# Optimization experiments

Hardware: AMD Instinct MI355X
Metric: run time of the kernel (lower is better)

The kernel has to match this reference:

```python
import jax, jax.numpy as jnp
import numpy as np

N, M, D, DV = 8192, 8192, 512, 512

def setup_inputs() -> dict:
    key = jax.random.key(0)
    kq, kk, kv = jax.random.split(key, 3)
    return {
        "query": jax.random.normal(kq, (N, D), dtype=jnp.float32),
        "key": jax.random.normal(kk, (M, D), dtype=jnp.float32),
        "value": jax.random.normal(kv, (M, DV), dtype=jnp.float32),
    }

def reference(query, key, value):
    # scores: [N, M] = Q @ K^T (no scale, no mask, matching the torch module)
    scores = query @ key.T
    attn = jax.nn.softmax(scores, axis=-1)
    return attn @ value
```

## Files before the change

kernel.cpp:

```cpp
#include <hip/hip_runtime.h>
#include <hip/hip_fp16.h>
#include <stdint.h>

typedef _Float16 f16;
typedef _Float16 f16x8 __attribute__((ext_vector_type(8)));
typedef float    f32x4 __attribute__((ext_vector_type(4)));
typedef int      i32x4 __attribute__((ext_vector_type(4)));

#define NQ 8192
#define NK 8192
#define DD 512
#define DVV 512

__device__ __forceinline__ void stage16(const void* g, void* ldsbase, int lane) {
#if __has_builtin(__builtin_amdgcn_global_load_lds)
  __builtin_amdgcn_global_load_lds((const __attribute__((address_space(1))) void*)g,
                                   (__attribute__((address_space(3))) void*)ldsbase, 16, 0, 0);
#else
  ((i32x4*)ldsbase)[lane] = *(const i32x4*)g;
#endif
}

__global__ void conv_hilo(const float* __restrict__ src, f16* __restrict__ hi,
                          f16* __restrict__ lo, int n8) {
  int i = blockIdx.x * 256 + threadIdx.x;
  if (i >= n8) return;
  const float4* s4 = (const float4*)src;
  float4 a = s4[2 * i], b = s4[2 * i + 1];
  float vv[8] = {a.x, a.y, a.z, a.w, b.x, b.y, b.z, b.w};
  f16 h8[8], l8[8];
#pragma unroll
  for (int j = 0; j < 8; ++j) {
    f16 h = (f16)vv[j];
    h8[j] = h;
    l8[j] = (f16)(vv[j] - (float)h);
  }
  *(f16x8*)(hi + (size_t)i * 8) = *(f16x8*)h8;
  *(f16x8*)(lo + (size_t)i * 8) = *(f16x8*)l8;
}

__global__ void conv_f16k(const float* __restrict__ src, f16* __restrict__ dst, int n8) {
  int i = blockIdx.x * 256 + threadIdx.x;
  if (i >= n8) return;
  const float4* s4 = (const float4*)src;
  float4 a = s4[2 * i], b = s4[2 * i + 1];
  float vv[8] = {a.x, a.y, a.z, a.w, b.x, b.y, b.z, b.w};
  f16 h8[8];
#pragma unroll
  for (int j = 0; j < 8; ++j) h8[j] = (f16)vv[j];
  *(f16x8*)(dst + (size_t)i * 8) = *(f16x8*)h8;
}

__global__ void conv_vT(const float* __restrict__ v, f16* __restrict__ vT) {
  __shared__ float t[64][65];
  int k0 = blockIdx.x * 64, d0 = blockIdx.y * 64;
#pragma unroll
  for (int e = 0; e < 16; ++e) {
    int idx = threadIdx.x + e * 256;
    int kr = idx >> 6, dc = idx & 63;
    t[kr][dc] = v[(size_t)(k0 + kr) * DVV + d0 + dc];
  }
  __syncthreads();
  int dl = threadIdx.x >> 2, seg = (threadIdx.x & 3) * 16;
  f16 tmp[16];
#pragma unroll
  for (int c = 0; c < 16; ++c) tmp[c] = (f16)t[seg + c][dl];
  f16* dst = vT + (size_t)(d0 + dl) * NK + k0 + seg;
  *(f16x8*)dst = *(f16x8*)tmp;
  *(f16x8*)(dst + 8) = *(f16x8*)(tmp + 8);
}

__global__ __launch_bounds__(512, 2) void qk_kernel(
    const f16* __restrict__ qhi, const f16* __restrict__ qlo,
    const f16* __restrict__ khi,
    f16* __restrict__ s16, float* __restrict__ pm, float* __restrict__ ps) {
  __shared__ f16 LS[3 * 3 * 8192];
  __shared__ float red[2][4][128];
  const int tid = threadIdx.x;
  const int lane = tid & 63, wid = tid >> 6;
  const int wr = wid >> 2, wc = wid & 3;
  const int bx = blockIdx.x, by = blockIdx.y;
  const int lo16 = lane & 15, hi4 = lane >> 4;
  const int swz = (lo16 & 3) ^ ((lo16 >> 2) & 3);
  const int u_s = hi4 ^ swz;

  f32x4 acc[8][4] = {};

  const f16* tp[3] = {qhi + (size_t)(by * 256) * DD, qlo + (size_t)(by * 256) * DD,
                      khi + (size_t)(bx * 256) * DD};
  const int srow4 = lane >> 2, usl = lane & 3;
  const f16* sptr[6];
  int dbase[6];
#pragma unroll
  for (int s2 = 0; s2 < 6; ++s2) {
    int u = wid + s2 * 8;
    int tt = u >> 4, rb = u & 15;
    int r = rb * 16 + srow4;
    int ug = usl ^ (r & 3) ^ ((r >> 2) & 3);
    sptr[s2] = tp[tt] + (size_t)r * DD + ug * 8;
    dbase[s2] = tt * 3 * 8192 + rb * 512;
  }
  f16* lsf = (f16*)LS;

#define STG(s2, t2, buf) stage16(sptr[s2] + (t2) * 32, lsf + dbase[s2] + (buf) * 8192, lane)

#pragma unroll
  for (int s2 = 0; s2 < 6; ++s2) STG(s2, 0, 0);
#pragma unroll
  for (int s2 = 0; s2 < 6; ++s2) STG(s2, 1, 1);
  asm volatile("s_waitcnt vmcnt(6)" ::: "memory");
  __builtin_amdgcn_s_barrier();
  asm volatile("" ::: "memory");

  const int abase = (wr * 128 + lo16) * 32 + u_s * 8;
  const int bbase = (wc * 64 + lo16) * 32 + u_s * 8;

  int cur = 0, pre = 2;
  for (int t = 0; t < 16; ++t) {
    const f16* Qh = lsf + cur * 8192;
    const f16* Ql = lsf + (3 + cur) * 8192;
    const f16* Kh = lsf + (6 + cur) * 8192;
    const bool st = (t <= 13);
    f16x8 bfr[4], ah[4], al[4];
#pragma unroll
    for (int j = 0; j < 4; ++j) bfr[j] = *(const f16x8*)&Kh[bbase + j * 512];
#pragma unroll
    for (int i = 0; i < 4; ++i) {
      ah[i] = *(const f16x8*)&Qh[abase + i * 512];
      al[i] = *(const f16x8*)&Ql[abase + i * 512];
    }
    if (st) { STG(0, t + 2, pre); STG(1, t + 2, pre); STG(2, t + 2, pre); }
    __builtin_amdgcn_s_barrier();
    asm volatile("" ::: "memory");
    __builtin_amdgcn_s_setprio(1);
#pragma unroll
    for (int i = 0; i < 4; ++i)
#pragma unroll
      for (int j = 0; j < 4; ++j) {
        acc[i][j] = __builtin_amdgcn_mfma_f32_16x16x32_f16(ah[i], bfr[j], acc[i][j], 0, 0, 0);
        acc[i][j] = __builtin_amdgcn_mfma_f32_16x16x32_f16(al[i], bfr[j], acc[i][j], 0, 0, 0);
      }
    __builtin_amdgcn_s_setprio(0);
    __builtin_amdgcn_s_barrier();
    asm volatile("" ::: "memory");
#pragma unroll
    for (int i = 0; i < 4; ++i) {
      ah[i] = *(const f16x8*)&Qh[abase + (4 + i) * 512];
      al[i] = *(const f16x8*)&Ql[abase + (4 + i) * 512];
    }
    if (st) { STG(3, t + 2, pre); STG(4, t + 2, pre); STG(5, t + 2, pre); }
    __builtin_amdgcn_s_barrier();
    asm volatile("" ::: "memory");
    __builtin_amdgcn_s_setprio(1);
#pragma unroll
    for (int i = 0; i < 4; ++i)
#pragma unroll
      for (int j = 0; j < 4; ++j) {
        acc[4 + i][j] = __builtin_amdgcn_mfma_f32_16x16x32_f16(ah[i], bfr[j], acc[4 + i][j], 0, 0, 0);
        acc[4 + i][j] = __builtin_amdgcn_mfma_f32_16x16x32_f16(al[i], bfr[j], acc[4 + i][j], 0, 0, 0);
      }
    __builtin_amdgcn_s_setprio(0);
    if (st) asm volatile("s_waitcnt vmcnt(6)" ::: "memory");
    else    asm volatile("s_waitcnt vmcnt(0)" ::: "memory");
    __builtin_amdgcn_s_barrier();
    asm volatile("" ::: "memory");
    cur = (cur == 2) ? 0 : cur + 1;
    pre = (pre == 2) ? 0 : pre + 1;
  }
#undef STG

  __syncthreads();
  float rmax[8][4];
#pragma unroll
  for (int i = 0; i < 8; ++i)
#pragma unroll
    for (int r = 0; r < 4; ++r) {
      float m = fmaxf(fmaxf(acc[i][0][r], acc[i][1][r]), fmaxf(acc[i][2][r], acc[i][3][r]));
#pragma unroll
      for (int d = 1; d < 16; d <<= 1) m = fmaxf(m, __shfl_xor(m, d, 64));
      rmax[i][r] = m;
    }
  if (lo16 == 0) {
#pragma unroll
    for (int i = 0; i < 8; ++i)
#pragma unroll
      for (int r = 0; r < 4; ++r) red[wr][wc][i * 16 + hi4 * 4 + r] = rmax[i][r];
  }
  __syncthreads();
  float pmv[8][4];
#pragma unroll
  for (int i = 0; i < 8; ++i)
#pragma unroll
    for (int r = 0; r < 4; ++r) {
      int rl = i * 16 + hi4 * 4 + r;
      pmv[i][r] = fmaxf(fmaxf(red[wr][0][rl], red[wr][1][rl]),
                        fmaxf(red[wr][2][rl], red[wr][3][rl]));
    }
  __syncthreads();
  float rsum[8][4];
#pragma unroll
  for (int i = 0; i < 8; ++i)
#pragma unroll
    for (int r = 0; r < 4; ++r) {
      float s = 0.f;
#pragma unroll
      for (int j = 0; j < 4; ++j) {
        float p = __expf(acc[i][j][r] - pmv[i][r]);
        acc[i][j][r] = p;
        s += p;
      }
#pragma unroll
      for (int d = 1; d < 16; d <<= 1) s += __shfl_xor(s, d, 64);
      rsum[i][r] = s;
    }
#pragma unroll
  for (int i = 0; i < 8; ++i)
#pragma unroll
    for (int r = 0; r < 4; ++r) {
      size_t grow = (size_t)(by * 256 + wr * 128 + i * 16 + hi4 * 4 + r);
#pragma unroll
      for (int j = 0; j < 4; ++j)
        s16[grow * NK + bx * 256 + wc * 64 + j * 16 + lo16] = (f16)acc[i][j][r];
    }
  if (lo16 == 0) {
#pragma unroll
    for (int i = 0; i < 8; ++i)
#pragma unroll
      for (int r = 0; r < 4; ++r) red[wr][wc][i * 16 + hi4 * 4 + r] = rsum[i][r];
  }
  __syncthreads();
  if (wc == 0 && lo16 == 0) {
#pragma unroll
    for (int i = 0; i < 8; ++i)
#pragma unroll
      for (int r = 0; r < 4; ++r) {
        int rl = i * 16 + hi4 * 4 + r;
        size_t grow = (size_t)(by * 256 + wr * 128 + rl);
        pm[grow * 32 + bx] = pmv[i][r];
        ps[grow * 32 + bx] = red[wr][0][rl] + red[wr][1][rl] + red[wr][2][rl] + red[wr][3][rl];
      }
  }
}

__global__ void red_kernel(const float* __restrict__ pm, const float* __restrict__ ps,
                           float* __restrict__ coef) {
  int row = blockIdx.x * 8 + (threadIdx.x >> 5);
  int t = threadIdx.x & 31;
  float pmt = pm[(size_t)row * 32 + t];
  float m = pmt;
#pragma unroll
  for (int d = 1; d < 32; d <<= 1) m = fmaxf(m, __shfl_xor(m, d, 32));
  float e = __expf(pmt - m);
  float l = ps[(size_t)row * 32 + t] * e;
#pragma unroll
  for (int d = 1; d < 32; d <<= 1) l += __shfl_xor(l, d, 32);
  coef[(size_t)row * 32 + t] = e / l;
}

__global__ __launch_bounds__(256, 2) void pv_kernel(
    const f16* __restrict__ p16, const float* __restrict__ coef,
    const f16* __restrict__ vT, float* __restrict__ dst,
    int steps, size_t zstride) {
  __shared__ f16 lsA[2][128 * 64];
  __shared__ f16 lsB[2][128 * 64];
  const int tid = threadIdx.x, lane = tid & 63, wid = tid >> 6;
  const int lo16 = lane & 15, hi4 = lane >> 4;
  const int wr = wid >> 1, wc = wid & 1;
  const int bx = blockIdx.x, by = blockIdx.y, bz = blockIdx.z;
  const int g0 = bz * steps;
  f32x4 acc[4][4] = {};

  const int arow0 = tid >> 3, acol = tid & 7;
  const int srw = lane >> 3;
  const int sc = (lane & 7) ^ srw;

  f16x8 va[4];
  float scv[4];

#pragma unroll
  for (int u = 0; u < 4; ++u)
    va[u] = *(const f16x8*)(p16 + (size_t)(by * 128 + u * 32 + arow0) * NK + (size_t)g0 * 64 + acol * 8);
#pragma unroll
  for (int i = 0; i < 4; ++i) {
    int unit = wid * 4 + i;
    int row = unit * 8 + srw;
    stage16(vT + (size_t)(bx * 128 + row) * NK + (size_t)g0 * 64 + sc * 8,
            &lsB[0][unit * 512], lane);
  }
#pragma unroll
  for (int u = 0; u < 4; ++u)
    scv[u] = coef[(size_t)(by * 128 + u * 32 + arow0) * 32 + (g0 >> 2)];
#pragma unroll
  for (int u = 0; u < 4; ++u) {
    int row = u * 32 + arow0;
    f16x8 vv = va[u] * (f16)scv[u];
    *(f16x8*)&lsA[0][row * 64 + ((acol ^ (row & 7)) << 3)] = vv;
  }
  __syncthreads();

  for (int s = 0; s < steps; ++s) {
    const int cur = s & 1, nxt = cur ^ 1;
    const int g = g0 + s;
    if (s + 1 < steps) {
#pragma unroll
      for (int u = 0; u < 4; ++u)
        va[u] = *(const f16x8*)(p16 + (size_t)(by * 128 + u * 32 + arow0) * NK +
                                (size_t)(g + 1) * 64 + acol * 8);
#pragma unroll
      for (int i = 0; i < 4; ++i) {
        int unit = wid * 4 + i;
        int row = unit * 8 + srw;
        stage16(vT + (size_t)(bx * 128 + row) * NK + (size_t)(g + 1) * 64 + sc * 8,
                &lsB[nxt][unit * 512], lane);
      }
#pragma unroll
      for (int u = 0; u < 4; ++u)
        scv[u] = coef[(size_t)(by * 128 + u * 32 + arow0) * 32 + ((g + 1) >> 2)];
    }
#pragma unroll
    for (int ks = 0; ks < 2; ++ks) {
      f16x8 af[4], bf[4];
#pragma unroll
      for (int i = 0; i < 4; ++i) {
        int row = wr * 64 + i * 16 + lo16;
        af[i] = *(const f16x8*)&lsA[cur][row * 64 + (((ks * 4 + hi4) ^ (row & 7)) << 3)];
      }
#pragma unroll
      for (int j = 0; j < 4; ++j) {
        int dv = wc * 64 + j * 16 + lo16;
        bf[j] = *(const f16x8*)&lsB[cur][dv * 64 + (((ks * 4 + hi4) ^ (dv & 7)) << 3)];
      }
#pragma unroll
      for (int i = 0; i < 4; ++i)
#pragma unroll
        for (int j = 0; j < 4; ++j)
          acc[i][j] = __builtin_amdgcn_mfma_f32_16x16x32_f16(af[i], bf[j], acc[i][j], 0, 0, 0);
    }
    if (s + 1 < steps) {
#pragma unroll
      for (int u = 0; u < 4; ++u) {
        int row = u * 32 + arow0;
        f16x8 vv = va[u] * (f16)scv[u];
        *(f16x8*)&lsA[nxt][row * 64 + ((acol ^ (row & 7)) << 3)] = vv;
      }
    }
    __syncthreads();
  }

  float* o = dst + (size_t)bz * zstride;
#pragma unroll
  for (int i = 0; i < 4; ++i)
#pragma unroll
    for (int j = 0; j < 4; ++j)
#pragma unroll
      for (int r = 0; r < 4; ++r)
        o[(size_t)(by * 128 + wr * 64 + i * 16 + hi4 * 4 + r) * DVV +
          bx * 128 + wc * 64 + j * 16 + lo16] = acc[i][j][r];
}

__global__ void reduce_out(const float* __restrict__ part, float* __restrict__ out,
                           int ks, size_t n4) {
  size_t i = (size_t)blockIdx.x * 256 + threadIdx.x;
  if (i >= n4) return;
  float4 a = ((const float4*)part)[i];
  for (int z = 1; z < ks; ++z) {
    float4 b = ((const float4*)(part + z * n4 * 4))[i];
    a.x += b.x; a.y += b.y; a.z += b.z; a.w += b.w;
  }
  ((float4*)out)[i] = a;
}

__global__ void zero_out(float* o, int n) {
  int i = blockIdx.x * 256 + threadIdx.x;
  if (i < n) o[i] = 0.f;
}

extern "C" void kernel_launch(void* const* d_in, const int* in_sizes, int n_in,
                              void* d_out, int out_size, void* d_ws, size_t ws_size,
                              hipStream_t stream) {
  (void)in_sizes; (void)n_in; (void)out_size;
  const float* Q = (const float*)d_in[0];
  const float* K = (const float*)d_in[1];
  const float* V = (const float*)d_in[2];
  float* out = (float*)d_out;

  const size_t sz16 = (size_t)NK * DD * 2;
  const size_t fixedB = 2 * sz16;
  const size_t perRow = 1024 * 2 + 128 * 3 + (size_t)NK * 2;
  const size_t partB = (size_t)16384 * DVV * 4;
  int nc = 0;
  for (int cand = 8192; cand >= 1024; cand >>= 1)
    if (fixedB + (size_t)cand * perRow + partB <= ws_size) { nc = cand; break; }
  if (nc == 0) {
    zero_out<<<(NQ * DVV + 255) / 256, 256, 0, stream>>>(out, NQ * DVV);
    return;
  }
  const int ks = 16384 / nc;
  const int steps = 128 / ks;

  char* w = (char*)d_ws;
  f16* khi = (f16*)w;
  f16* vT = (f16*)(w + sz16);
  char* p = w + fixedB;
  f16* qhi = (f16*)p;      p += (size_t)nc * 1024;
  f16* qlo = (f16*)p;      p += (size_t)nc * 1024;
  float* pm = (float*)p;   p += (size_t)nc * 128;
  float* ps = (float*)p;   p += (size_t)nc * 128;
  float* coef = (float*)p; p += (size_t)nc * 128;
  f16* s16 = (f16*)p;      p += (size_t)nc * NK * 2;
  float* part = (float*)p;

  conv_f16k<<<NK * DD / 8 / 256, 256, 0, stream>>>(K, khi, NK * DD / 8);
  conv_vT<<<dim3(NK / 64, DVV / 64), 256, 0, stream>>>(V, vT);

  for (int c = 0; c < NQ / nc; ++c) {
    conv_hilo<<<nc * DD / 8 / 256, 256, 0, stream>>>(Q + (size_t)c * nc * DD, qhi, qlo, nc * DD / 8);
    qk_kernel<<<dim3(NK / 256, nc / 256), 512, 0, stream>>>(qhi, qlo, khi, s16, pm, ps);
    red_kernel<<<nc / 8, 256, 0, stream>>>(pm, ps, coef);
    pv_kernel<<<dim3(DVV / 128, nc / 128, ks), 256, 0, stream>>>(
        s16, coef, vT, part, steps, (size_t)nc * DVV);
    reduce_out<<<(int)(((size_t)nc * DVV / 4 + 255) / 256), 256, 0, stream>>>(
        part, out + (size_t)c * nc * DVV, ks, (size_t)nc * DVV / 4);
  }
}
```

Before: 303.5 us.

## Drop Q hi/lo split, use plain fp16 Q and restructure QK staging

Removes the hi/lo fp16 split of Q, so QK^T uses a single fp16 product instead of two MFMAs per tile pair. The QK main loop moves from a 3-buffer, 32-wide K-step pipeline to a 2-buffer, 64-wide K-step pipeline with an XOR-swizzled LDS layout. This halves the QK MFMA work and the Q conversion traffic. It gives up the extra precision in the scores, which get exponentiated without scaling, so accuracy near tolerance is at risk.

```diff
diff --git a/kernel.cpp b/kernel.cpp
--- a/kernel.cpp
+++ b/kernel.cpp
@@ -21,24 +21,6 @@
 #endif
 }
 
-__global__ void conv_hilo(const float* __restrict__ src, f16* __restrict__ hi,
-                          f16* __restrict__ lo, int n8) {
-  int i = blockIdx.x * 256 + threadIdx.x;
-  if (i >= n8) return;
-  const float4* s4 = (const float4*)src;
-  float4 a = s4[2 * i], b = s4[2 * i + 1];
-  float vv[8] = {a.x, a.y, a.z, a.w, b.x, b.y, b.z, b.w};
-  f16 h8[8], l8[8];
-#pragma unroll
-  for (int j = 0; j < 8; ++j) {
-    f16 h = (f16)vv[j];
-    h8[j] = h;
-    l8[j] = (f16)(vv[j] - (float)h);
-  }
-  *(f16x8*)(hi + (size_t)i * 8) = *(f16x8*)h8;
-  *(f16x8*)(lo + (size_t)i * 8) = *(f16x8*)l8;
-}
-
 __global__ void conv_f16k(const float* __restrict__ src, f16* __restrict__ dst, int n8) {
   int i = blockIdx.x * 256 + threadIdx.x;
   if (i >= n8) return;
@@ -71,105 +53,90 @@
 }
 
 __global__ __launch_bounds__(512, 2) void qk_kernel(
-    const f16* __restrict__ qhi, const f16* __restrict__ qlo,
-    const f16* __restrict__ khi,
+    const f16* __restrict__ q16, const f16* __restrict__ k16,
     f16* __restrict__ s16, float* __restrict__ pm, float* __restrict__ ps) {
-  __shared__ f16 LS[3 * 3 * 8192];
+  __shared__ f16 LS[2 * 2 * 16384];
   __shared__ float red[2][4][128];
-  const int tid = threadIdx.x;
-  const int lane = tid & 63, wid = tid >> 6;
+  const int tid = threadIdx.x, lane = tid & 63, wid = tid >> 6;
   const int wr = wid >> 2, wc = wid & 3;
   const int bx = blockIdx.x, by = blockIdx.y;
   const int lo16 = lane & 15, hi4 = lane >> 4;
-  const int swz = (lo16 & 3) ^ ((lo16 >> 2) & 3);
-  const int u_s = hi4 ^ swz;
 
   f32x4 acc[8][4] = {};
 
-  const f16* tp[3] = {qhi + (size_t)(by * 256) * DD, qlo + (size_t)(by * 256) * DD,
-                      khi + (size_t)(bx * 256) * DD};
-  const int srow4 = lane >> 2, usl = lane & 3;
-  const f16* sptr[6];
-  int dbase[6];
-#pragma unroll
-  for (int s2 = 0; s2 < 6; ++s2) {
-    int u = wid + s2 * 8;
-    int tt = u >> 4, rb = u & 15;
-    int r = rb * 16 + srow4;
-    int ug = usl ^ (r & 3) ^ ((r >> 2) & 3);
-    sptr[s2] = tp[tt] + (size_t)r * DD + ug * 8;
-    dbase[s2] = tt * 3 * 8192 + rb * 512;
-  }
-  f16* lsf = (f16*)LS;
-
-#define STG(s2, t2, buf) stage16(sptr[s2] + (t2) * 32, lsf + dbase[s2] + (buf) * 8192, lane)
-
-#pragma unroll
-  for (int s2 = 0; s2 < 6; ++s2) STG(s2, 0, 0);
-#pragma unroll
-  for (int s2 = 0; s2 < 6; ++s2) STG(s2, 1, 1);
-  asm volatile("s_waitcnt vmcnt(6)" ::: "memory");
+  const int srw = lane >> 3, sc8 = (lane & 7) ^ srw;
+  const f16* aptr[4]; const f16* bptr[4]; int adst[4], bdst[4];
+#pragma unroll
+  for (int u = 0; u < 4; ++u) {
+    int r = wid * 32 + u * 8 + srw;
+    aptr[u] = q16 + (size_t)(by * 256 + r) * DD + sc8 * 8;
+    bptr[u] = k16 + (size_t)(bx * 256 + r) * DD + sc8 * 8;
+    adst[u] = (wid * 32 + u * 8) * 64;
+    bdst[u] = adst[u] + 16384;
+  }
+  int aoff[8][2], boff[4][2];
+#pragma unroll
+  for (int m = 0; m < 8; ++m)
+#pragma unroll
+    for (int kk = 0; kk < 2; ++kk) {
+      int row = wr * 128 + m * 16 + lo16;
+      aoff[m][kk] = row * 64 + (((kk * 4 + hi4) ^ (row & 7)) << 3);
+    }
+#pragma unroll
+  for (int n = 0; n < 4; ++n)
+#pragma unroll
+    for (int kk = 0; kk < 2; ++kk) {
+      int row = wc * 64 + n * 16 + lo16;
+      boff[n][kk] = 16384 + row * 64 + (((kk * 4 + hi4) ^ (row & 7)) << 3);
+    }
+
+#define STG(t2, buf)                                                        \
+  do {                                                                      \
+    _Pragma("unroll") for (int u = 0; u < 4; ++u) {                         \
+      stage16(aptr[u] + (t2) * 64, LS + (buf) * 32768 + adst[u], lane);     \
+      stage16(bptr[u] + (t2) * 64, LS + (buf) * 32768 + bdst[u], lane);     \
+    }                                                                       \
+  } while (0)
+
+  STG(0, 0);
+  asm volatile("s_waitcnt vmcnt(0)" ::: "memory");
   __builtin_amdgcn_s_barrier();
   asm volatile("" ::: "memory");
 
-  const int abase = (wr * 128 + lo16) * 32 + u_s * 8;
-  const int bbase = (wc * 64 + lo16) * 32 + u_s * 8;
-
-  int cur = 0, pre = 2;
-  for (int t = 0; t < 16; ++t) {
-    const f16* Qh = lsf + cur * 8192;
-    const f16* Ql = lsf + (3 + cur) * 8192;
-    const f16* Kh = lsf + (6 + cur) * 8192;
-    const bool st = (t <= 13);
-    f16x8 bfr[4], ah[4], al[4];
-#pragma unroll
-    for (int j = 0; j < 4; ++j) bfr[j] = *(const f16x8*)&Kh[bbase + j * 512];
-#pragma unroll
-    for (int i = 0; i < 4; ++i) {
-      ah[i] = *(const f16x8*)&Qh[abase + i * 512];
-      al[i] = *(const f16x8*)&Ql[abase + i * 512];
-    }
-    if (st) { STG(0, t + 2, pre); STG(1, t + 2, pre); STG(2, t + 2, pre); }
+  for (int t = 0; t < 8; ++t) {
+    const int cur = t & 1;
+    if (t < 7) STG(t + 1, cur ^ 1);
+    const f16* Bb = LS + cur * 32768;
+    f16x8 bf[2][4];
+#pragma unroll
+    for (int n = 0; n < 4; ++n)
+#pragma unroll
+      for (int kk = 0; kk < 2; ++kk) bf[kk][n] = *(const f16x8*)&Bb[boff[n][kk]];
+#pragma unroll
+    for (int h = 0; h < 2; ++h) {
+      f16x8 af[4][2];
+#pragma unroll
+      for (int mi = 0; mi < 4; ++mi)
+#pragma unroll
+        for (int kk = 0; kk < 2; ++kk) af[mi][kk] = *(const f16x8*)&Bb[aoff[h * 4 + mi][kk]];
+      __builtin_amdgcn_s_setprio(1);
+#pragma unroll
+      for (int mi = 0; mi < 4; ++mi)
+#pragma unroll
+        for (int n = 0; n < 4; ++n) {
+          acc[h * 4 + mi][n] =
+              __builtin_amdgcn_mfma_f32_16x16x32_f16(af[mi][0], bf[0][n], acc[h * 4 + mi][n], 0, 0, 0);
+          acc[h * 4 + mi][n] =
+              __builtin_amdgcn_mfma_f32_16x16x32_f16(af[mi][1], bf[1][n], acc[h * 4 + mi][n], 0, 0, 0);
+        }
+      __builtin_amdgcn_s_setprio(0);
+    }
+    asm volatile("s_waitcnt vmcnt(0)" ::: "memory");
     __builtin_amdgcn_s_barrier();
     asm volatile("" ::: "memory");
-    __builtin_amdgcn_s_setprio(1);
-#pragma unroll
-    for (int i = 0; i < 4; ++i)
-#pragma unroll
-      for (int j = 0; j < 4; ++j) {
-        acc[i][j] = __builtin_amdgcn_mfma_f32_16x16x32_f16(ah[i], bfr[j], acc[i][j], 0, 0, 0);
-        acc[i][j] = __builtin_amdgcn_mfma_f32_16x16x32_f16(al[i], bfr[j], acc[i][j], 0, 0, 0);
-      }
-    __builtin_amdgcn_s_setprio(0);
-    __builtin_amdgcn_s_barrier();
-    asm volatile("" ::: "memory");
-#pragma unroll
-    for (int i = 0; i < 4; ++i) {
-      ah[i] = *(const f16x8*)&Qh[abase + (4 + i) * 512];
-      al[i] = *(const f16x8*)&Ql[abase + (4 + i) * 512];
-    }
-    if (st) { STG(3, t + 2, pre); STG(4, t + 2, pre); STG(5, t + 2, pre); }
-    __builtin_amdgcn_s_barrier();
-    asm volatile("" ::: "memory");
-    __builtin_amdgcn_s_setprio(1);
-#pragma unroll
-    for (int i = 0; i < 4; ++i)
-#pragma unroll
-      for (int j = 0; j < 4; ++j) {
-        acc[4 + i][j] = __builtin_amdgcn_mfma_f32_16x16x32_f16(ah[i], bfr[j], acc[4 + i][j], 0, 0, 0);
-        acc[4 + i][j] = __builtin_amdgcn_mfma_f32_16x16x32_f16(al[i], bfr[j], acc[4 + i][j], 0, 0, 0);
-      }
-    __builtin_amdgcn_s_setprio(0);
-    if (st) asm volatile("s_waitcnt vmcnt(6)" ::: "memory");
-    else    asm volatile("s_waitcnt vmcnt(0)" ::: "memory");
-    __builtin_amdgcn_s_barrier();
-    asm volatile("" ::: "memory");
-    cur = (cur == 2) ? 0 : cur + 1;
-    pre = (pre == 2) ? 0 : pre + 1;
   }
 #undef STG
 
-  __syncthreads();
   float rmax[8][4];
 #pragma unroll
   for (int i = 0; i < 8; ++i)
@@ -386,7 +353,7 @@
 
   const size_t sz16 = (size_t)NK * DD * 2;
   const size_t fixedB = 2 * sz16;
-  const size_t perRow = 1024 * 2 + 128 * 3 + (size_t)NK * 2;
+  const size_t perRow = 1024 + 128 * 3 + (size_t)NK * 2;
   const size_t partB = (size_t)16384 * DVV * 4;
   int nc = 0;
   for (int cand = 8192; cand >= 1024; cand >>= 1)
@@ -399,23 +366,22 @@
   const int steps = 128 / ks;
 
   char* w = (char*)d_ws;
-  f16* khi = (f16*)w;
+  f16* k16 = (f16*)w;
   f16* vT = (f16*)(w + sz16);
   char* p = w + fixedB;
-  f16* qhi = (f16*)p;      p += (size_t)nc * 1024;
-  f16* qlo = (f16*)p;      p += (size_t)nc * 1024;
+  f16* q16 = (f16*)p;      p += (size_t)nc * 1024;
   float* pm = (float*)p;   p += (size_t)nc * 128;
   float* ps = (float*)p;   p += (size_t)nc * 128;
   float* coef = (float*)p; p += (size_t)nc * 128;
   f16* s16 = (f16*)p;      p += (size_t)nc * NK * 2;
   float* part = (float*)p;
 
-  conv_f16k<<<NK * DD / 8 / 256, 256, 0, stream>>>(K, khi, NK * DD / 8);
+  conv_f16k<<<NK * DD / 8 / 256, 256, 0, stream>>>(K, k16, NK * DD / 8);
   conv_vT<<<dim3(NK / 64, DVV / 64), 256, 0, stream>>>(V, vT);
 
   for (int c = 0; c < NQ / nc; ++c) {
-    conv_hilo<<<nc * DD / 8 / 256, 256, 0, stream>>>(Q + (size_t)c * nc * DD, qhi, qlo, nc * DD / 8);
-    qk_kernel<<<dim3(NK / 256, nc / 256), 512, 0, stream>>>(qhi, qlo, khi, s16, pm, ps);
+    conv_f16k<<<nc * DD / 8 / 256, 256, 0, stream>>>(Q + (size_t)c * nc * DD, q16, nc * DD / 8);
+    qk_kernel<<<dim3(NK / 256, nc / 256), 512, 0, stream>>>(q16, k16, s16, pm, ps);
     red_kernel<<<nc / 8, 256, 0, stream>>>(pm, ps, coef);
     pv_kernel<<<dim3(DVV / 128, nc / 128, ks), 256, 0, stream>>>(
         s16, coef, vT, part, steps, (size_t)nc * DVV);
```

New measurement: 244.6 us. -19.4%, faster.
